# Performance work log

Measured on AMD Instinct MI355X. Metric: run time of the kernel, lower is better.

Reference implementation:

```python
import jax, jax.numpy as jnp
import numpy as np

IN_DIM = 8192
OUT_DIM = 8192
BATCH = 2048


def setup_inputs() -> dict:
    key = jax.random.key(0)
    k1, k2, k3, k4 = jax.random.split(key, 4)
    x = jax.random.uniform(k1, (BATCH, IN_DIM), dtype=jnp.float32)  # soft bits in [0,1]
    weights = jax.random.normal(k2, (OUT_DIM, 16), dtype=jnp.float32)
    idx_a = jax.random.randint(k3, (OUT_DIM,), 0, IN_DIM, dtype=jnp.int64)
    idx_b = jax.random.randint(k4, (OUT_DIM,), 0, IN_DIM, dtype=jnp.int64)
    return {"x": x, "weights": weights, "idx_a": idx_a, "idx_b": idx_b}


def _gate_values(a, b):
    # The 16 real-valued relaxations of the 2-input binary logic gates.
    ab = a * b
    return [
        jnp.zeros_like(a),      # 0:  False
        ab,                     # 1:  a AND b
        a - ab,                 # 2:  a AND NOT b
        a,                      # 3:  a
        b - ab,                 # 4:  NOT a AND b
        b,                      # 5:  b
        a + b - 2.0 * ab,       # 6:  a XOR b
        a + b - ab,             # 7:  a OR b
        1.0 - (a + b - ab),     # 8:  NOT (a OR b)
        1.0 - (a + b - 2.0 * ab),  # 9: NOT (a XOR b)
        1.0 - b,                # 10: NOT b
        1.0 - b + ab,           # 11: a OR NOT b
        1.0 - a,                # 12: NOT a
        1.0 - a + ab,           # 13: NOT a OR b
        1.0 - ab,               # 14: NOT (a AND b)
        jnp.ones_like(a),       # 15: True
    ]


def reference(x, weights, idx_a, idx_b):
    # training=True path of LogicLayer.forward_python
    a = x[:, idx_a]  # [B, OUT]
    b = x[:, idx_b]  # [B, OUT]
    w = jax.nn.softmax(weights, axis=-1)  # [OUT, 16]
    gates = _gate_values(a, b)
    out = jnp.zeros_like(a)
    for k in range(16):  # fixed small structural loop over the 16 gates
        out = out + w[None, :, k] * gates[k]
    return out
```

## Files before the change

kernel.cpp:

```cpp
#include <hip/hip_runtime.h>

#define IN_DIM 8192
#define OUT_DIM 8192
#define BATCH 2048

#define TPB 512
#define JT 2
#define JTILE (OUT_DIM / JT)
#define OPT (JTILE / TPB / 4)
#define RROWS 8
#define SVEC (IN_DIM / 4 / TPB)

typedef float fvec4 __attribute__((ext_vector_type(4)));

#define BAR() __asm__ __volatile__("s_waitcnt lgkmcnt(0)\n\ts_barrier" ::: "memory")

__global__ __launch_bounds__(256) void coeff_kernel(
    const float* __restrict__ w,
    float* __restrict__ c0, float* __restrict__ ca,
    float* __restrict__ cb, float* __restrict__ cab)
{
    int j = blockIdx.x * blockDim.x + threadIdx.x;
    if (j >= OUT_DIM) return;

    const float* wj = w + (size_t)j * 16;
    float wv[16];
    float m = -1e30f;
#pragma unroll
    for (int k = 0; k < 16; ++k) { wv[k] = wj[k]; m = fmaxf(m, wv[k]); }
    float s = 0.f;
#pragma unroll
    for (int k = 0; k < 16; ++k) { wv[k] = __expf(wv[k] - m); s += wv[k]; }
    float inv = 1.0f / s;
#pragma unroll
    for (int k = 0; k < 16; ++k) wv[k] *= inv;

    c0[j]  = wv[8] + wv[9] + wv[10] + wv[11] + wv[12] + wv[13] + wv[14] + wv[15];
    ca[j]  = wv[2] + wv[3] + wv[6] + wv[7] - wv[8] - wv[9] - wv[12] - wv[13];
    cb[j]  = wv[4] + wv[5] + wv[6] + wv[7] - wv[8] - wv[9] - wv[10] - wv[11];
    cab[j] = wv[1] - wv[2] - wv[4] - 2.f * wv[6] - wv[7]
           + wv[8] + 2.f * wv[9] + wv[11] + wv[13] - wv[14];
}

__global__ __launch_bounds__(TPB, 4) void logic_kernel(
    const float* __restrict__ x,
    const int* __restrict__ idx_a,
    const int* __restrict__ idx_b,
    const float* __restrict__ c0, const float* __restrict__ ca,
    const float* __restrict__ cb, const float* __restrict__ cab,
    float* __restrict__ out)
{
    __shared__ float xrow[2][IN_DIM];

    const int jt    = blockIdx.x & (JT - 1);
    const int rg    = blockIdx.x / JT;
    const int row0  = rg * RROWS;
    const int jb4   = jt * (JTILE / 4);
    const int tid   = threadIdx.x;

    const int4*   ia4  = (const int4*)idx_a;
    const int4*   ib4  = (const int4*)idx_b;
    const float4* c04  = (const float4*)c0;
    const float4* ca4  = (const float4*)ca;
    const float4* cb4  = (const float4*)cb;
    const float4* cab4 = (const float4*)cab;

    int4   ia[OPT], ib[OPT];
    float4 v0[OPT], va[OPT], vb[OPT], vab[OPT];
#pragma unroll
    for (int it = 0; it < OPT; ++it) {
        int j4  = jb4 + it * TPB + tid;
        ia[it]  = ia4[j4];
        ib[it]  = ib4[j4];
        v0[it]  = c04[j4];
        va[it]  = ca4[j4];
        vb[it]  = cb4[j4];
        vab[it] = cab4[j4];
    }

    float4 pf[SVEC];
    {
        const float4* xr4 = (const float4*)(x + (size_t)row0 * IN_DIM);
#pragma unroll
        for (int k = 0; k < SVEC; ++k) pf[k] = xr4[k * TPB + tid];
    }

    for (int r = 0; r < RROWS; ++r) {
        float4* buf4 = (float4*)xrow[r & 1];
#pragma unroll
        for (int k = 0; k < SVEC; ++k) buf4[k * TPB + tid] = pf[k];

        if (r + 1 < RROWS) {
            const float4* xr4 = (const float4*)(x + (size_t)(row0 + r + 1) * IN_DIM);
#pragma unroll
            for (int k = 0; k < SVEC; ++k) pf[k] = xr4[k * TPB + tid];
        }

        BAR();

        const float* xr = xrow[r & 1];
        fvec4* out4 = (fvec4*)(out + (size_t)(row0 + r) * OUT_DIM);
#pragma unroll
        for (int it = 0; it < OPT; ++it) {
            int j4 = jb4 + it * TPB + tid;

            float a0 = xr[ia[it].x], b0 = xr[ib[it].x];
            float a1 = xr[ia[it].y], b1 = xr[ib[it].y];
            float a2 = xr[ia[it].z], b2 = xr[ib[it].z];
            float a3 = xr[ia[it].w], b3 = xr[ib[it].w];

            fvec4 o;
            o.x = v0[it].x + va[it].x * a0 + vb[it].x * b0 + vab[it].x * (a0 * b0);
            o.y = v0[it].y + va[it].y * a1 + vb[it].y * b1 + vab[it].y * (a1 * b1);
            o.z = v0[it].z + va[it].z * a2 + vb[it].z * b2 + vab[it].z * (a2 * b2);
            o.w = v0[it].w + va[it].w * a3 + vb[it].w * b3 + vab[it].w * (a3 * b3);
            __builtin_nontemporal_store(o, &out4[j4]);
        }
    }
}

extern "C" void kernel_launch(void* const* d_in, const int* in_sizes, int n_in,
                              void* d_out, int out_size, void* d_ws, size_t ws_size,
                              hipStream_t stream)
{
    const float* x       = (const float*)d_in[0];
    const float* weights = (const float*)d_in[1];
    const int*   idx_a   = (const int*)d_in[2];
    const int*   idx_b   = (const int*)d_in[3];
    float* out = (float*)d_out;

    float* wsF = (float*)d_ws;
    float* c0  = wsF;
    float* ca  = wsF + OUT_DIM;
    float* cb  = wsF + 2 * OUT_DIM;
    float* cab = wsF + 3 * OUT_DIM;

    coeff_kernel<<<OUT_DIM / 256, 256, 0, stream>>>(weights, c0, ca, cb, cab);
    logic_kernel<<<JT * (BATCH / RROWS), TPB, 0, stream>>>(
        x, idx_a, idx_b, c0, ca, cb, cab, out);
}
```

Measured before the change: 129.2 us.

## Pack gather indices and fp16 coefficients to cut registers, single-buffer LDS

The coefficient kernel now packs idx_a/idx_b into one 32-bit word and stores the four gate coefficients as two half2 pairs, so each logic thread holds 3 int4 per tile instead of 6 vectors. The x-row shared buffer drops from double to single, with an extra barrier before each overwrite. RROWS is halved and launch bounds raised to 8 waves. The aim is higher occupancy and fewer coefficient loads. The cost is fp16 rounding of the coefficients, which could break tolerance, and extra per-row barriers.

```diff
diff --git a/kernel.cpp b/kernel.cpp
--- a/kernel.cpp
+++ b/kernel.cpp
@@ -1,4 +1,5 @@
 #include <hip/hip_runtime.h>
+#include <hip/hip_fp16.h>
 
 #define IN_DIM 8192
 #define OUT_DIM 8192
@@ -8,17 +9,20 @@
 #define JT 2
 #define JTILE (OUT_DIM / JT)
 #define OPT (JTILE / TPB / 4)
-#define RROWS 8
+#define RROWS 4
 #define SVEC (IN_DIM / 4 / TPB)
 
 typedef float fvec4 __attribute__((ext_vector_type(4)));
 
-#define BAR() __asm__ __volatile__("s_waitcnt lgkmcnt(0)\n\ts_barrier" ::: "memory")
+#define BAR_LGKM() __asm__ __volatile__("s_waitcnt lgkmcnt(0)\n\ts_barrier" ::: "memory")
 
 __global__ __launch_bounds__(256) void coeff_kernel(
     const float* __restrict__ w,
-    float* __restrict__ c0, float* __restrict__ ca,
-    float* __restrict__ cb, float* __restrict__ cab)
+    const int* __restrict__ idx_a,
+    const int* __restrict__ idx_b,
+    int* __restrict__ pidx,
+    __half2* __restrict__ pc1,
+    __half2* __restrict__ pc2)
 {
     int j = blockIdx.x * blockDim.x + threadIdx.x;
     if (j >= OUT_DIM) return;
@@ -35,47 +39,43 @@
 #pragma unroll
     for (int k = 0; k < 16; ++k) wv[k] *= inv;
 
-    c0[j]  = wv[8] + wv[9] + wv[10] + wv[11] + wv[12] + wv[13] + wv[14] + wv[15];
-    ca[j]  = wv[2] + wv[3] + wv[6] + wv[7] - wv[8] - wv[9] - wv[12] - wv[13];
-    cb[j]  = wv[4] + wv[5] + wv[6] + wv[7] - wv[8] - wv[9] - wv[10] - wv[11];
-    cab[j] = wv[1] - wv[2] - wv[4] - 2.f * wv[6] - wv[7]
-           + wv[8] + 2.f * wv[9] + wv[11] + wv[13] - wv[14];
+    float c0  = wv[8] + wv[9] + wv[10] + wv[11] + wv[12] + wv[13] + wv[14] + wv[15];
+    float ca  = wv[2] + wv[3] + wv[6] + wv[7] - wv[8] - wv[9] - wv[12] - wv[13];
+    float cb  = wv[4] + wv[5] + wv[6] + wv[7] - wv[8] - wv[9] - wv[10] - wv[11];
+    float cab = wv[1] - wv[2] - wv[4] - 2.f * wv[6] - wv[7]
+              + wv[8] + 2.f * wv[9] + wv[11] + wv[13] - wv[14];
+
+    pidx[j] = (idx_a[j] & 0xffff) | (idx_b[j] << 16);
+    pc1[j]  = __floats2half2_rn(c0, ca);
+    pc2[j]  = __floats2half2_rn(cb, cab);
 }
 
-__global__ __launch_bounds__(TPB, 4) void logic_kernel(
+__global__ __launch_bounds__(TPB, 8) void logic_kernel(
     const float* __restrict__ x,
-    const int* __restrict__ idx_a,
-    const int* __restrict__ idx_b,
-    const float* __restrict__ c0, const float* __restrict__ ca,
-    const float* __restrict__ cb, const float* __restrict__ cab,
+    const int* __restrict__ pidx,
+    const __half2* __restrict__ pc1,
+    const __half2* __restrict__ pc2,
     float* __restrict__ out)
 {
-    __shared__ float xrow[2][IN_DIM];
+    __shared__ float xrow[IN_DIM];
 
-    const int jt    = blockIdx.x & (JT - 1);
-    const int rg    = blockIdx.x / JT;
-    const int row0  = rg * RROWS;
-    const int jb4   = jt * (JTILE / 4);
-    const int tid   = threadIdx.x;
+    const int jt   = blockIdx.x & (JT - 1);
+    const int rg   = blockIdx.x / JT;
+    const int row0 = rg * RROWS;
+    const int jb4  = jt * (JTILE / 4);
+    const int tid  = threadIdx.x;
 
-    const int4*   ia4  = (const int4*)idx_a;
-    const int4*   ib4  = (const int4*)idx_b;
-    const float4* c04  = (const float4*)c0;
-    const float4* ca4  = (const float4*)ca;
-    const float4* cb4  = (const float4*)cb;
-    const float4* cab4 = (const float4*)cab;
+    const int4* pidx4 = (const int4*)pidx;
+    const int4* pc14  = (const int4*)pc1;
+    const int4* pc24  = (const int4*)pc2;
 
-    int4   ia[OPT], ib[OPT];
-    float4 v0[OPT], va[OPT], vb[OPT], vab[OPT];
+    int4 pi[OPT], h1[OPT], h2[OPT];
 #pragma unroll
     for (int it = 0; it < OPT; ++it) {
-        int j4  = jb4 + it * TPB + tid;
-        ia[it]  = ia4[j4];
-        ib[it]  = ib4[j4];
-        v0[it]  = c04[j4];
-        va[it]  = ca4[j4];
-        vb[it]  = cb4[j4];
-        vab[it] = cab4[j4];
+        int j4 = jb4 + it * TPB + tid;
+        pi[it] = pidx4[j4];
+        h1[it] = pc14[j4];
+        h2[it] = pc24[j4];
     }
 
     float4 pf[SVEC];
@@ -85,8 +85,11 @@
         for (int k = 0; k < SVEC; ++k) pf[k] = xr4[k * TPB + tid];
     }
 
+#pragma unroll
     for (int r = 0; r < RROWS; ++r) {
-        float4* buf4 = (float4*)xrow[r & 1];
+        BAR_LGKM();
+
+        float4* buf4 = (float4*)xrow;
 #pragma unroll
         for (int k = 0; k < SVEC; ++k) buf4[k * TPB + tid] = pf[k];
 
@@ -96,24 +99,33 @@
             for (int k = 0; k < SVEC; ++k) pf[k] = xr4[k * TPB + tid];
         }
 
-        BAR();
+        BAR_LGKM();
 
-        const float* xr = xrow[r & 1];
         fvec4* out4 = (fvec4*)(out + (size_t)(row0 + r) * OUT_DIM);
 #pragma unroll
         for (int it = 0; it < OPT; ++it) {
             int j4 = jb4 + it * TPB + tid;
 
-            float a0 = xr[ia[it].x], b0 = xr[ib[it].x];
-            float a1 = xr[ia[it].y], b1 = xr[ib[it].y];
-            float a2 = xr[ia[it].z], b2 = xr[ib[it].z];
-            float a3 = xr[ia[it].w], b3 = xr[ib[it].w];
+            int i0 = pi[it].x, i1 = pi[it].y, i2 = pi[it].z, i3 = pi[it].w;
+            float a0 = xrow[i0 & 0xffff], b0 = xrow[i0 >> 16];
+            float a1 = xrow[i1 & 0xffff], b1 = xrow[i1 >> 16];
+            float a2 = xrow[i2 & 0xffff], b2 = xrow[i2 >> 16];
+            float a3 = xrow[i3 & 0xffff], b3 = xrow[i3 >> 16];
+
+            float2 f10 = __half22float2(*(const __half2*)&h1[it].x);
+            float2 f11 = __half22float2(*(const __half2*)&h1[it].y);
+            float2 f12 = __half22float2(*(const __half2*)&h1[it].z);
+            float2 f13 = __half22float2(*(const __half2*)&h1[it].w);
+            float2 f20 = __half22float2(*(const __half2*)&h2[it].x);
+            float2 f21 = __half22float2(*(const __half2*)&h2[it].y);
+            float2 f22 = __half22float2(*(const __half2*)&h2[it].z);
+            float2 f23 = __half22float2(*(const __half2*)&h2[it].w);
 
             fvec4 o;
-            o.x = v0[it].x + va[it].x * a0 + vb[it].x * b0 + vab[it].x * (a0 * b0);
-            o.y = v0[it].y + va[it].y * a1 + vb[it].y * b1 + vab[it].y * (a1 * b1);
-            o.z = v0[it].z + va[it].z * a2 + vb[it].z * b2 + vab[it].z * (a2 * b2);
-            o.w = v0[it].w + va[it].w * a3 + vb[it].w * b3 + vab[it].w * (a3 * b3);
+            o.x = f10.x + f10.y * a0 + f20.x * b0 + f20.y * (a0 * b0);
+            o.y = f11.x + f11.y * a1 + f21.x * b1 + f21.y * (a1 * b1);
+            o.z = f12.x + f12.y * a2 + f22.x * b2 + f22.y * (a2 * b2);
+            o.w = f13.x + f13.y * a3 + f23.x * b3 + f23.y * (a3 * b3);
             __builtin_nontemporal_store(o, &out4[j4]);
         }
     }
@@ -129,13 +141,10 @@
     const int*   idx_b   = (const int*)d_in[3];
     float* out = (float*)d_out;
 
-    float* wsF = (float*)d_ws;
-    float* c0  = wsF;
-    float* ca  = wsF + OUT_DIM;
-    float* cb  = wsF + 2 * OUT_DIM;
-    float* cab = wsF + 3 * OUT_DIM;
+    int*     pidx = (int*)d_ws;
+    __half2* pc1  = (__half2*)(pidx + OUT_DIM);
+    __half2* pc2  = pc1 + OUT_DIM;
 
-    coeff_kernel<<<OUT_DIM / 256, 256, 0, stream>>>(weights, c0, ca, cb, cab);
-    logic_kernel<<<JT * (BATCH / RROWS), TPB, 0, stream>>>(
-        x, idx_a, idx_b, c0, ca, cb, cab, out);
+    coeff_kernel<<<OUT_DIM / 256, 256, 0, stream>>>(weights, idx_a, idx_b, pidx, pc1, pc2);
+    logic_kernel<<<JT * (BATCH / RROWS), TPB, 0, stream>>>(x, pidx, pc1, pc2, out);
 }
```

Result: slower. 147.2 us (+13.9%).
